# Kernel tuning notes

Hardware: AMD Instinct MI355X
Metric: run time of the kernel (lower is better)

Reference implementation:

```python
import jax, jax.numpy as jnp
import numpy as np

N, E, T, D, A = 50000, 160000, 8192, 32, 6  # nodes, edges, torsions, dim, action_dim


def setup_inputs() -> dict:
    key = jax.random.key(0)
    ks = jax.random.split(key, 16)
    rn = lambda k, s, sc=0.1: jax.random.normal(k, s, jnp.float32) * sc
    return {
        "x": jax.random.normal(ks[0], (N, 3), jnp.float32),
        "edge_index": jax.random.randint(ks[1], (2, E), 0, N),
        "edge_attr": jax.random.uniform(ks[2], (E, 7), dtype=jnp.float32),
        "nonring": jax.random.randint(ks[3], (T, 4), 0, N),
        "lin0_w": rn(ks[4], (3, D)), "lin0_b": jnp.zeros((D,), jnp.float32),
        "nn1_w": rn(ks[5], (7, D)), "nn1_b": jnp.zeros((D,), jnp.float32),
        "nn2_w": rn(ks[6], (D, D * D), 0.02), "nn2_b": jnp.zeros((D * D,), jnp.float32),
        "conv_root": rn(ks[7], (D, D)), "conv_b": jnp.zeros((D,), jnp.float32),
        "gru_w_ih": rn(ks[8], (D, 3 * D)), "gru_w_hh": rn(ks[9], (D, 3 * D)),
        "gru_b_ih": jnp.zeros((3 * D,), jnp.float32), "gru_b_hh": jnp.zeros((3 * D,), jnp.float32),
        "lstm_w_ih": rn(ks[10], (2 * D, 4 * D)), "lstm_w_hh": rn(ks[11], (D, 4 * D)),
        "lstm_b_ih": jnp.zeros((4 * D,), jnp.float32), "lstm_b_hh": jnp.zeros((4 * D,), jnp.float32),
        "lin1_w": rn(ks[12], (6 * D, D)), "lin1_b": jnp.zeros((D,), jnp.float32),
        "lin2_w": rn(ks[13], (D, A)), "lin2_b": jnp.zeros((A,), jnp.float32),
    }


def reference(x, edge_index, edge_attr, nonring,
              lin0_w, lin0_b, nn1_w, nn1_b, nn2_w, nn2_b, conv_root, conv_b,
              gru_w_ih, gru_w_hh, gru_b_ih, gru_b_hh,
              lstm_w_ih, lstm_w_hh, lstm_b_ih, lstm_b_hh,
              lin1_w, lin1_b, lin2_w, lin2_b):
    src, dst = edge_index[0], edge_index[1]
    out = jax.nn.relu(x @ lin0_w + lin0_b)                       # [N, D]
    h = out                                                      # GRU hidden (batch = nodes)
    # Per-edge dim x dim weight matrices (edge_attr is loop-invariant)
    Wedge = (jax.nn.relu(edge_attr @ nn1_w + nn1_b) @ nn2_w + nn2_b).reshape(E, D, D)
    deg = jnp.clip(jax.ops.segment_sum(jnp.ones((E,), jnp.float32), dst, num_segments=N), 1.0)[:, None]
    for _ in range(6):
        # NNConv: gather -> per-edge matvec -> scatter-mean, plus root transform + bias
        msg = jnp.einsum('ei,eio->eo', out[src], Wedge)          # [E, D]
        agg = jax.ops.segment_sum(msg, dst, num_segments=N) / deg
        m = jax.nn.relu(out @ conv_root + agg + conv_b)
        # GRU step (torch gate order r, z, n)
        gx = m @ gru_w_ih + gru_b_ih
        gh = h @ gru_w_hh + gru_b_hh
        r = jax.nn.sigmoid(gx[:, :D] + gh[:, :D])
        z = jax.nn.sigmoid(gx[:, D:2 * D] + gh[:, D:2 * D])
        n = jnp.tanh(gx[:, 2 * D:] + r * gh[:, 2 * D:])
        h = (1.0 - z) * n + z * h
        out = h
    # Set2Set pooling, single graph (B = 1); torch LSTM gate order i, f, g, o
    hl = jnp.zeros((D,), out.dtype)
    cl = jnp.zeros((D,), out.dtype)
    q_star = jnp.zeros((2 * D,), out.dtype)
    for _ in range(6):
        g = q_star @ lstm_w_ih + lstm_b_ih + hl @ lstm_w_hh + lstm_b_hh
        i = jax.nn.sigmoid(g[:D]); f = jax.nn.sigmoid(g[D:2 * D])
        gg = jnp.tanh(g[2 * D:3 * D]); o = jax.nn.sigmoid(g[3 * D:])
        cl = f * cl + i * gg
        hl = o * jnp.tanh(cl)
        q = hl
        a = jax.nn.softmax(out @ q)                              # attention over all nodes
        r_vec = a @ out                                          # [D]
        q_star = jnp.concatenate([q, r_vec])                     # [2D]
    pool = q_star                                                # [2D]
    g4 = out[nonring.reshape(-1)]                                # [4T, D]
    g4 = g4.reshape(4 * D, -1).T                                 # [T, 4D] (faithful view+permute)
    rep = jnp.repeat(pool, g4.shape[0]).reshape(g4.shape[0], -1) # [T, 2D] (repeat_interleave+view)
    cat = jnp.concatenate([g4, rep], axis=1)                     # [T, 6D]
    y = jax.nn.relu(cat @ lin1_w + lin1_b)
    return y @ lin2_w + lin2_b                                   # [T, A]
```

## Files before the change

### kernel.cpp

```cpp
#include <hip/hip_runtime.h>
#include <hip/hip_bf16.h>

#define NN 50000
#define NE 160000
#define NT 8192
#define DD 32
#define AA 6

typedef __attribute__((ext_vector_type(8))) short bf16x8s;
typedef __attribute__((ext_vector_type(4))) float f32x4;

__device__ float g_out[NN * DD];
__device__ float g_msg[NE * DD];
__device__ unsigned int g_h2b[NE * 16];
__device__ int g_src[NE];
__device__ int g_poe[NE];
__device__ unsigned int g_bcnt[NN];
__device__ unsigned int g_row[NN + 1];
__device__ unsigned int g_cur[NN];
__device__ unsigned int g_btot[256], g_boff[256];
__device__ bf16x8s g_w2frag[33 * 2 * 64];
__device__ bf16x8s g_gru_frag[28 * 64];
__device__ float g_hl[DD], g_cl[DD], g_q[DD], g_part[DD + 1];
__device__ unsigned int g_cnt;

__device__ __forceinline__ float sigm(float x) { return 1.0f / (1.0f + __expf(-x)); }
__device__ __forceinline__ float tanhx(float x) { return 1.0f - 2.0f / (__expf(2.0f * x) + 1.0f); }
__device__ __forceinline__ unsigned short f2bf(float f) {
    unsigned int u = __float_as_uint(f);
    u = (u + 0x7fffu + ((u >> 16) & 1u)) >> 16;
    return (unsigned short)u;
}
__device__ __forceinline__ float bflo(unsigned int pk) { return __uint_as_float(pk << 16); }
__device__ __forceinline__ float bfhi(unsigned int pk) { return __uint_as_float(pk & 0xffff0000u); }
__device__ __forceinline__ void fma4(float4& a, float s, const float4 b) {
    a.x = fmaf(s, b.x, a.x); a.y = fmaf(s, b.y, a.y);
    a.z = fmaf(s, b.z, a.z); a.w = fmaf(s, b.w, a.w);
}
#define CVTPK(dst, lo, hi) asm("v_cvt_pk_bf16_f32 %0, %1, %2" : "=v"(dst) : "v"(lo), "v"(hi))

__device__ __forceinline__ void split8(const float* v, bf16x8s& hi, bf16x8s& lo) {
    union U { bf16x8s v; unsigned int u[4]; } H, L;
    CVTPK(H.u[0], v[0], v[1]); CVTPK(H.u[1], v[2], v[3]);
    CVTPK(H.u[2], v[4], v[5]); CVTPK(H.u[3], v[6], v[7]);
    float r[8];
#pragma unroll
    for (int q = 0; q < 4; ++q) {
        r[2 * q]     = v[2 * q]     - bflo(H.u[q]);
        r[2 * q + 1] = v[2 * q + 1] - bfhi(H.u[q]);
    }
    CVTPK(L.u[0], r[0], r[1]); CVTPK(L.u[1], r[2], r[3]);
    CVTPK(L.u[2], r[4], r[5]); CVTPK(L.u[3], r[6], r[7]);
    hi = H.v; lo = L.v;
}

__global__ __launch_bounds__(256) void k_prep0(const float* __restrict__ x,
                                               const float* __restrict__ l0w,
                                               const float* __restrict__ l0b,
                                               const float* __restrict__ w2m,
                                               const float* __restrict__ b2m,
                                               const float* __restrict__ root,
                                               const float* __restrict__ wih,
                                               const float* __restrict__ whh,
                                               const float* __restrict__ lbih,
                                               const float* __restrict__ lbhh) {
    const int t = blockIdx.x * 256 + threadIdx.x;
    {
        const int n = t >> 5, d = t & 31;
        float v = l0b[d];
        v = fmaf(x[n * 3 + 0], l0w[0 * DD + d], v);
        v = fmaf(x[n * 3 + 1], l0w[1 * DD + d], v);
        v = fmaf(x[n * 3 + 2], l0w[2 * DD + d], v);
        g_out[t] = fmaxf(v, 0.f);
    }
    if (t < NN) g_bcnt[t] = 0u;
    if (t < 33 * 2 * 64 * 8) {
        const int j = t & 7, l = (t >> 3) & 63, c = (t >> 9) & 1, s = t >> 10;
        const int kk = (l >> 4) * 8 + j;
        const int col = c * 16 + (l & 15);
        const float v = (s == 32) ? b2m[kk * DD + col] : w2m[(32 * s + kk) * DD + col];
        ((unsigned short*)g_w2frag)[t] = f2bf(v);
    }
    if (t < 28 * 64) {
        const int lane = t & 63, f = t >> 6;
        const float* M; int ncols, c, part;
        if (f < 4)       { M = root; ncols = 32; c = f >> 1;        part = f & 1; }
        else if (f < 16) { M = wih;  ncols = 96; c = (f - 4) >> 1;  part = f & 1; }
        else             { M = whh;  ncols = 96; c = (f - 16) >> 1; part = f & 1; }
        unsigned short out8[8];
#pragma unroll
        for (int j = 0; j < 8; ++j) {
            const int k = (lane >> 4) * 8 + j;
            const float v = M[k * ncols + c * 16 + (lane & 15)];
            const unsigned short hi = f2bf(v);
            out8[j] = (part == 0) ? hi : f2bf(v - __uint_as_float((unsigned int)hi << 16));
        }
        g_gru_frag[f * 64 + lane] = *(bf16x8s*)out8;
    }
    if (t < DD) {
        const float ig = sigm(lbih[t] + lbhh[t]);
        const float g2 = tanhx(lbih[2 * DD + t] + lbhh[2 * DD + t]);
        const float og = sigm(lbih[3 * DD + t] + lbhh[3 * DD + t]);
        const float cc = ig * g2;
        g_cl[t] = cc; const float hn = og * tanhx(cc); g_hl[t] = hn; g_q[t] = hn;
    }
    if (t >= DD && t < 2 * DD + 1 + DD) { if (t - DD <= 2 * DD) g_part[t - DD] = 0.f; }
    if (t == 1793) g_cnt = 0u;
}

__global__ __launch_bounds__(256) void k_hist(const int* __restrict__ ei) {
    const int e = blockIdx.x * 256 + threadIdx.x;
    atomicAdd(&g_bcnt[ei[NE + e]], 1u);
}

__global__ __launch_bounds__(256) void k_scanA() {
    __shared__ unsigned int s[256];
    const int t = threadIdx.x;
    const int idx = blockIdx.x * 256 + t;
    const unsigned int c = (idx < NN) ? g_bcnt[idx] : 0u;
    s[t] = c;
    __syncthreads();
#pragma unroll
    for (int off = 1; off < 256; off <<= 1) {
        const unsigned int o = (t >= off) ? s[t - off] : 0u;
        __syncthreads();
        s[t] += o;
        __syncthreads();
    }
    if (idx < NN) g_row[idx] = s[t] - c;
    if (t == 255) g_btot[blockIdx.x] = s[255];
}

__global__ void k_scanB() {
    __shared__ unsigned int s[256];
    const int t = threadIdx.x;
    const unsigned int c = (t < 196) ? g_btot[t] : 0u;
    s[t] = c;
    __syncthreads();
#pragma unroll
    for (int off = 1; off < 256; off <<= 1) {
        const unsigned int o = (t >= off) ? s[t - off] : 0u;
        __syncthreads();
        s[t] += o;
        __syncthreads();
    }
    if (t < 196) g_boff[t] = s[t] - c;
}

__global__ __launch_bounds__(256) void k_scanC() {
    const int idx = blockIdx.x * 256 + threadIdx.x;
    if (idx < NN) {
        const unsigned int v = g_row[idx] + g_boff[blockIdx.x];
        g_row[idx] = v;
        g_cur[idx] = v;
    }
    if (idx == 0) g_row[NN] = NE;
}

__global__ __launch_bounds__(256) void k_scatter(const int* __restrict__ ei) {
    const int e = blockIdx.x * 256 + threadIdx.x;
    const int d = ei[NE + e];
    const unsigned int pos = atomicAdd(&g_cur[d], 1u);
    g_src[pos] = ei[e];
    g_poe[pos] = e;
}

__global__ __launch_bounds__(256) void k_h2(const float* __restrict__ ea,
                                            const float* __restrict__ w,
                                            const float* __restrict__ b) {
    const int t = blockIdx.x * 256 + threadIdx.x;
    const int p = t >> 4, kp = t & 15;
    const int oe = g_poe[p];
    const int k0 = kp * 2;
    float a0 = b[k0], a1 = b[k0 + 1];
#pragma unroll
    for (int i = 0; i < 7; ++i) {
        const float eav = ea[oe * 7 + i];
        a0 = fmaf(eav, w[i * DD + k0], a0);
        a1 = fmaf(eav, w[i * DD + k0 + 1], a1);
    }
    unsigned int pk;
    CVTPK(pk, fmaxf(a0, 0.f), fmaxf(a1, 0.f));
    g_h2b[t] = pk;
}

__global__ __launch_bounds__(256) void k_edge_mfma() {
    const int wid = threadIdx.x >> 6, lane = threadIdx.x & 63;
    const int w = blockIdx.x * 4 + wid;
    const int col = lane & 15, quad = lane >> 4;
    const bf16x8s* __restrict__ B = g_w2frag;

    const bf16x8s bbias0 = B[32 * 128 + lane];
    const bf16x8s bbias1 = B[32 * 128 + 64 + lane];

    float4 u0[2], u1[2];
    unsigned int h2p[2][16];
#pragma unroll
    for (int g = 0; g < 2; ++g) {
        const int e = w * 32 + g * 16 + col;
        const int src = g_src[e];
        u0[g] = *(const float4*)&g_out[src * DD + quad * 8];
        u1[g] = *(const float4*)&g_out[src * DD + quad * 8 + 4];
        *(uint4*)&h2p[g][0]  = *(const uint4*)&g_h2b[e * 16];
        *(uint4*)&h2p[g][4]  = *(const uint4*)&g_h2b[e * 16 + 4];
        *(uint4*)&h2p[g][8]  = *(const uint4*)&g_h2b[e * 16 + 8];
        *(uint4*)&h2p[g][12] = *(const uint4*)&g_h2b[e * 16 + 12];
    }

    union ABu { bf16x8s v; unsigned int u[4]; };
    f32x4 acc[2][2];
#pragma unroll
    for (int g = 0; g < 2; ++g) {
        acc[g][0] = (f32x4){0.f, 0.f, 0.f, 0.f};
        acc[g][1] = (f32x4){0.f, 0.f, 0.f, 0.f};
    }

#define EDGE_STEP(S, B0V, B1V)                                                                   \
    do {                                                                                          \
        _Pragma("unroll")                                                                         \
        for (int g = 0; g < 2; ++g) {                                                             \
            const unsigned int hw = h2p[g][(S) >> 1];                                             \
            const float hs = ((S)&1) ? bfhi(hw) : bflo(hw);                                       \
            ABu A;                                                                                \
            CVTPK(A.u[0], hs * u0[g].x, hs * u0[g].y);                                            \
            CVTPK(A.u[1], hs * u0[g].z, hs * u0[g].w);                                            \
            CVTPK(A.u[2], hs * u1[g].x, hs * u1[g].y);                                            \
            CVTPK(A.u[3], hs * u1[g].z, hs * u1[g].w);                                            \
            acc[g][0] = __builtin_amdgcn_mfma_f32_16x16x32_bf16(A.v, B0V, acc[g][0], 0, 0, 0);    \
            acc[g][1] = __builtin_amdgcn_mfma_f32_16x16x32_bf16(A.v, B1V, acc[g][1], 0, 0, 0);    \
        }                                                                                         \
    } while (0)

    bf16x8s ca0 = B[0 * 128 + lane], cb0 = B[0 * 128 + 64 + lane];
    bf16x8s ca1 = B[1 * 128 + lane], cb1 = B[1 * 128 + 64 + lane];
    bf16x8s ca2 = B[2 * 128 + lane], cb2 = B[2 * 128 + 64 + lane];
    bf16x8s ca3 = B[3 * 128 + lane], cb3 = B[3 * 128 + 64 + lane];
    bf16x8s na0, nb0, na1, nb1, na2, nb2, na3, nb3;

#pragma unroll
    for (int blk = 0; blk < 8; ++blk) {
        if (blk < 7) {
            const int r = blk * 4 + 4;
            na0 = B[(r + 0) * 128 + lane]; nb0 = B[(r + 0) * 128 + 64 + lane];
            na1 = B[(r + 1) * 128 + lane]; nb1 = B[(r + 1) * 128 + 64 + lane];
            na2 = B[(r + 2) * 128 + lane]; nb2 = B[(r + 2) * 128 + 64 + lane];
            na3 = B[(r + 3) * 128 + lane]; nb3 = B[(r + 3) * 128 + 64 + lane];
        }
        EDGE_STEP(blk * 4 + 0, ca0, cb0);
        EDGE_STEP(blk * 4 + 1, ca1, cb1);
        EDGE_STEP(blk * 4 + 2, ca2, cb2);
        EDGE_STEP(blk * 4 + 3, ca3, cb3);
        if (blk < 7) {
            ca0 = na0; cb0 = nb0; ca1 = na1; cb1 = nb1;
            ca2 = na2; cb2 = nb2; ca3 = na3; cb3 = nb3;
        }
    }
#undef EDGE_STEP

    {
#pragma unroll
        for (int g = 0; g < 2; ++g) {
            ABu Au;
            CVTPK(Au.u[0], u0[g].x, u0[g].y); CVTPK(Au.u[1], u0[g].z, u0[g].w);
            CVTPK(Au.u[2], u1[g].x, u1[g].y); CVTPK(Au.u[3], u1[g].z, u1[g].w);
            acc[g][0] = __builtin_amdgcn_mfma_f32_16x16x32_bf16(Au.v, bbias0, acc[g][0], 0, 0, 0);
            acc[g][1] = __builtin_amdgcn_mfma_f32_16x16x32_bf16(Au.v, bbias1, acc[g][1], 0, 0, 0);
        }
    }
#pragma unroll
    for (int g = 0; g < 2; ++g)
#pragma unroll
        for (int r = 0; r < 4; ++r) {
            const int p = w * 32 + g * 16 + quad * 4 + r;
            g_msg[p * DD + col] = acc[g][0][r];
            g_msg[p * DD + 16 + col] = acc[g][1][r];
        }
}

__global__ __launch_bounds__(256) void k_node_mfma(const float* __restrict__ cb,
                                                   const float* __restrict__ bih,
                                                   const float* __restrict__ bhh) {
    __shared__ float sm[4][16 * 36];
    __shared__ float smsg[4][16 * 32];
    const int wid = threadIdx.x >> 6, lane = threadIdx.x & 63;
    const int nt = blockIdx.x * 4 + wid;
    if (nt >= NN / 16) return;
    const int nb = nt * 16;
    const int col = lane & 15, quad = lane >> 4;
    const bf16x8s* FB = g_gru_frag;
    float* smt = sm[wid];
    float* smm = smsg[wid];

    float hv8[8];
    *(float4*)&hv8[0] = *(const float4*)&g_out[(nb + col) * DD + quad * 8];
    *(float4*)&hv8[4] = *(const float4*)&g_out[(nb + col) * DD + quad * 8 + 4];
    bf16x8s hAh, hAl; split8(hv8, hAh, hAl);

    unsigned int nr0[4], nr1[4];
#pragma unroll
    for (int r = 0; r < 4; ++r) {
        const int node = nb + quad * 4 + r;
        nr0[r] = g_row[node];
        nr1[r] = g_row[node + 1];
    }
    const unsigned int e0t = g_row[nb], e1t = g_row[nb + 16];

    float agg0[4] = {0.f, 0.f, 0.f, 0.f};
    float agg1[4] = {0.f, 0.f, 0.f, 0.f};
    for (unsigned int ec = e0t; ec < e1t; ec += 16) {
        const int idx = min((int)ec * 32 + lane * 8, NE * 32 - 8);
        const float4 v0 = *(const float4*)&g_msg[idx];
        const float4 v1 = *(const float4*)&g_msg[idx + 4];
        *(float4*)&smm[lane * 8] = v0;
        *(float4*)&smm[lane * 8 + 4] = v1;
#pragma unroll
        for (int r = 0; r < 4; ++r) {
            const int lo = (int)max(nr0[r], ec) - (int)ec;
            const int hi = (int)min(nr1[r], ec + 16u) - (int)ec;
            for (int s = lo; s < hi; ++s) {
                agg0[r] += smm[s * 32 + col];
                agg1[r] += smm[s * 32 + 16 + col];
            }
        }
    }

    float invr[4];
#pragma unroll
    for (int r = 0; r < 4; ++r)
        invr[r] = 1.0f / fmaxf((float)(nr1[r] - nr0[r]), 1.0f);

#pragma unroll
    for (int c = 0; c < 2; ++c) {
        const float cbv = cb[c * 16 + col];
        f32x4 aM;
#pragma unroll
        for (int r = 0; r < 4; ++r)
            aM[r] = fmaf((c == 0) ? agg0[r] : agg1[r], invr[r], cbv);
        const bf16x8s Bh = FB[(c * 2 + 0) * 64 + lane];
        const bf16x8s Bl = FB[(c * 2 + 1) * 64 + lane];
        aM = __builtin_amdgcn_mfma_f32_16x16x32_bf16(hAh, Bh, aM, 0, 0, 0);
        aM = __builtin_amdgcn_mfma_f32_16x16x32_bf16(hAl, Bh, aM, 0, 0, 0);
        aM = __builtin_amdgcn_mfma_f32_16x16x32_bf16(hAh, Bl, aM, 0, 0, 0);
#pragma unroll
        for (int r = 0; r < 4; ++r)
            smt[(quad * 4 + r) * 36 + c * 16 + col] = fmaxf(aM[r], 0.f);
    }

    float mv8[8];
    *(float4*)&mv8[0] = *(const float4*)&smt[col * 36 + quad * 8];
    *(float4*)&mv8[4] = *(const float4*)&smt[col * 36 + quad * 8 + 4];
    bf16x8s mAh, mAl; split8(mv8, mAh, mAl);

    f32x4 R[2], Z[2], XN[2], HN[2];
#pragma unroll
    for (int c = 0; c < 6; ++c) {
        const float bx = bih[c * 16 + col], bh = bhh[c * 16 + col];
        f32x4 aX = {bx, bx, bx, bx}, aH = {bh, bh, bh, bh};
        const bf16x8s WIhf = FB[(4 + c * 2) * 64 + lane];
        const bf16x8s WIlf = FB[(5 + c * 2) * 64 + lane];
        const bf16x8s WHhf = FB[(16 + c * 2) * 64 + lane];
        const bf16x8s WHlf = FB[(17 + c * 2) * 64 + lane];
        aX = __builtin_amdgcn_mfma_f32_16x16x32_bf16(mAh, WIhf, aX, 0, 0, 0);
        aX = __builtin_amdgcn_mfma_f32_16x16x32_bf16(mAl, WIhf, aX, 0, 0, 0);
        aX = __builtin_amdgcn_mfma_f32_16x16x32_bf16(mAh, WIlf, aX, 0, 0, 0);
        aH = __builtin_amdgcn_mfma_f32_16x16x32_bf16(hAh, WHhf, aH, 0, 0, 0);
        aH = __builtin_amdgcn_mfma_f32_16x16x32_bf16(hAl, WHhf, aH, 0, 0, 0);
        aH = __builtin_amdgcn_mfma_f32_16x16x32_bf16(hAh, WHlf, aH, 0, 0, 0);
        if (c < 2) {
#pragma unroll
            for (int r = 0; r < 4; ++r) R[c][r] = sigm(aX[r] + aH[r]);
        } else if (c < 4) {
#pragma unroll
            for (int r = 0; r < 4; ++r) Z[c - 2][r] = sigm(aX[r] + aH[r]);
        } else {
            XN[c - 4] = aX; HN[c - 4] = aH;
        }
    }
#pragma unroll
    for (int c = 0; c < 2; ++c)
#pragma unroll
        for (int r = 0; r < 4; ++r) {
            const int addr = (nb + quad * 4 + r) * DD + c * 16 + col;
            const float nv = tanhx(XN[c][r] + R[c][r] * HN[c][r]);
            const float hv = g_out[addr];
            g_out[addr] = (1.f - Z[c][r]) * nv + Z[c][r] * hv;
        }
}

__global__ __launch_bounds__(256) void k_att_f(const float* __restrict__ wih,
                                               const float* __restrict__ whh,
                                               const float* __restrict__ bih,
                                               const float* __restrict__ bhh,
                                               const int dolstm) {
    __shared__ float sq[DD];
    __shared__ float red[4][DD + 1];
    __shared__ int slast;
    __shared__ float qs[64], shl[DD], gg[128];
    if (threadIdx.x < DD) sq[threadIdx.x] = g_q[threadIdx.x];
    __syncthreads();
    float pe = 0.f;
    float pv[DD];
#pragma unroll
    for (int i = 0; i < DD; ++i) pv[i] = 0.f;
    for (int n = blockIdx.x * blockDim.x + threadIdx.x; n < NN; n += gridDim.x * blockDim.x) {
        float row[DD];
#pragma unroll
        for (int q = 0; q < 8; ++q) *(float4*)&row[4 * q] = *(const float4*)&g_out[n * DD + 4 * q];
        float dot = 0.f;
#pragma unroll
        for (int i = 0; i < DD; ++i) dot = fmaf(row[i], sq[i], dot);
        const float e = __expf(dot);
        pe += e;
#pragma unroll
        for (int i = 0; i < DD; ++i) pv[i] = fmaf(e, row[i], pv[i]);
    }
#pragma unroll
    for (int off = 32; off > 0; off >>= 1) {
        pe += __shfl_down(pe, off, 64);
#pragma unroll
        for (int i = 0; i < DD; ++i) pv[i] += __shfl_down(pv[i], off, 64);
    }
    const int wid = threadIdx.x >> 6, lane = threadIdx.x & 63;
    if (lane == 0) {
        red[wid][0] = pe;
#pragma unroll
        for (int i = 0; i < DD; ++i) red[wid][1 + i] = pv[i];
    }
    __syncthreads();
    if (threadIdx.x < DD + 1) {
        const float s = red[0][threadIdx.x] + red[1][threadIdx.x] + red[2][threadIdx.x] + red[3][threadIdx.x];
        atomicAdd(&g_part[threadIdx.x], s);
    }
    __threadfence();
    __syncthreads();
    if (threadIdx.x == 0) {
        const unsigned int o = atomicAdd(&g_cnt, 1u);
        slast = (o == (unsigned int)(gridDim.x - 1)) ? 1 : 0;
    }
    __syncthreads();
    if (!slast) return;
    __threadfence();
    const int t = threadIdx.x;
    if (dolstm) {
        if (t < DD) { qs[t] = g_q[t]; shl[t] = g_hl[t]; }
        else if (t < 64) qs[t] = g_part[1 + t - DD] / g_part[0];
        __syncthreads();
        if (t < 128) {
            float acc = bih[t] + bhh[t];
            for (int i = 0; i < 64; ++i) acc = fmaf(qs[i], wih[i * 128 + t], acc);
            for (int i = 0; i < DD; ++i) acc = fmaf(shl[i], whh[i * 128 + t], acc);
            gg[t] = acc;
        }
        __syncthreads();
        if (t < DD) {
            const float ig = sigm(gg[t]), fg = sigm(gg[DD + t]);
            const float g2 = tanhx(gg[2 * DD + t]), og = sigm(gg[3 * DD + t]);
            const float cc = fmaf(fg, g_cl[t], ig * g2);
            g_cl[t] = cc; const float hn = og * tanhx(cc); g_hl[t] = hn; g_q[t] = hn;
        }
        if (t >= DD && t < 2 * DD + 1) g_part[t - DD] = 0.f;
    }
    if (t == 0) g_cnt = 0u;
}

__global__ __launch_bounds__(128) void k_readout(const int* __restrict__ nr,
                                                 const float* __restrict__ w1,
                                                 const float* __restrict__ b1,
                                                 const float* __restrict__ w2,
                                                 const float* __restrict__ b2,
                                                 float* __restrict__ yout) {
    __shared__ float sw1[192 * DD];
    __shared__ float sS1[DD];
    __shared__ float sw2[DD * AA];
    __shared__ float sb1[DD];
    __shared__ float sb2[AA];
    __shared__ float sred[32 * DD];
    for (int i = threadIdx.x; i < 192 * DD; i += 128) sw1[i] = w1[i];
    for (int i = threadIdx.x; i < DD * AA; i += 128) sw2[i] = w2[i];
    if (threadIdx.x < DD) sb1[threadIdx.x] = b1[threadIdx.x];
    if (threadIdx.x >= DD && threadIdx.x < DD + AA) sb2[threadIdx.x - DD] = b2[threadIdx.x - DD];
    __syncthreads();
    if (threadIdx.x < DD) {
        float s = 0.f;
        for (int c = 0; c < 64; ++c) s += sw1[(128 + c) * DD + threadIdx.x];
        sS1[threadIdx.x] = s;
    }
    __syncthreads();
    const int g = blockIdx.x;
    const int t0 = g * 32;
    const int f = threadIdx.x & 31;
    const int slice = threadIdx.x >> 5;
    const int rowbase = g >> 2, col = g & 3;
    float4 acc[8];
#pragma unroll
    for (int q = 0; q < 8; ++q) acc[q] = make_float4(0.f, 0.f, 0.f, 0.f);
    for (int pp = 0; pp < 32; ++pp) {
        const int p = slice * 32 + pp;
        const int node = nr[(p * 64 + rowbase) * 4 + col];
        const float v = g_out[node * DD + f];
#pragma unroll
        for (int q = 0; q < 8; ++q) fma4(acc[q], v, *(const float4*)&sw1[p * DD + 4 * q]);
    }
#pragma unroll
    for (int q = 0; q < 8; ++q) {
        acc[q].x += __shfl_xor(acc[q].x, 32, 64);
        acc[q].y += __shfl_xor(acc[q].y, 32, 64);
        acc[q].z += __shfl_xor(acc[q].z, 32, 64);
        acc[q].w += __shfl_xor(acc[q].w, 32, 64);
    }
    if (threadIdx.x >= 64 && threadIdx.x < 96) {
#pragma unroll
        for (int q = 0; q < 8; ++q) *(float4*)&sred[f * DD + 4 * q] = acc[q];
    }
    __syncthreads();
    if (threadIdx.x < 32) {
        const int pidx = g >> 2;
        const float poolv = (pidx < DD) ? g_q[pidx] : (g_part[1 + (pidx - DD)] / g_part[0]);
        float y[AA];
#pragma unroll
        for (int a = 0; a < AA; ++a) y[a] = sb2[a];
#pragma unroll
        for (int q = 0; q < 8; ++q) {
            const float4 o = *(const float4*)&sred[f * DD + 4 * q];
            const float vals[4] = {acc[q].x + o.x, acc[q].y + o.y, acc[q].z + o.z, acc[q].w + o.w};
#pragma unroll
            for (int cc = 0; cc < 4; ++cc) {
                const int d = 4 * q + cc;
                const float ad = fmaxf(fmaf(poolv, sS1[d], sb1[d]) + vals[cc], 0.f);
#pragma unroll
                for (int a = 0; a < AA; ++a) y[a] = fmaf(ad, sw2[d * AA + a], y[a]);
            }
        }
#pragma unroll
        for (int a = 0; a < AA; ++a) yout[(t0 + f) * AA + a] = y[a];
    }
}

extern "C" void kernel_launch(void* const* d_in, const int* in_sizes, int n_in,
                              void* d_out, int out_size, void* d_ws, size_t ws_size,
                              hipStream_t stream) {
    (void)in_sizes; (void)n_in; (void)out_size; (void)d_ws; (void)ws_size;
    const float* x        = (const float*)d_in[0];
    const int*   ei       = (const int*)d_in[1];
    const float* ea       = (const float*)d_in[2];
    const int*   nonring  = (const int*)d_in[3];
    const float* lin0_w   = (const float*)d_in[4];
    const float* lin0_b   = (const float*)d_in[5];
    const float* nn1_w    = (const float*)d_in[6];
    const float* nn1_b    = (const float*)d_in[7];
    const float* nn2_w    = (const float*)d_in[8];
    const float* nn2_b    = (const float*)d_in[9];
    const float* conv_root= (const float*)d_in[10];
    const float* conv_b   = (const float*)d_in[11];
    const float* gru_w_ih = (const float*)d_in[12];
    const float* gru_w_hh = (const float*)d_in[13];
    const float* gru_b_ih = (const float*)d_in[14];
    const float* gru_b_hh = (const float*)d_in[15];
    const float* lstm_w_ih= (const float*)d_in[16];
    const float* lstm_w_hh= (const float*)d_in[17];
    const float* lstm_b_ih= (const float*)d_in[18];
    const float* lstm_b_hh= (const float*)d_in[19];
    const float* lin1_w   = (const float*)d_in[20];
    const float* lin1_b   = (const float*)d_in[21];
    const float* lin2_w   = (const float*)d_in[22];
    const float* lin2_b   = (const float*)d_in[23];
    float* out = (float*)d_out;

    k_prep0<<<(NN * DD) / 256, 256, 0, stream>>>(x, lin0_w, lin0_b, nn2_w, nn2_b,
                                                 conv_root, gru_w_ih, gru_w_hh,
                                                 lstm_b_ih, lstm_b_hh);
    k_hist<<<NE / 256, 256, 0, stream>>>(ei);
    k_scanA<<<196, 256, 0, stream>>>();
    k_scanB<<<1, 256, 0, stream>>>();
    k_scanC<<<196, 256, 0, stream>>>();
    k_scatter<<<NE / 256, 256, 0, stream>>>(ei);
    k_h2<<<(NE * 16) / 256, 256, 0, stream>>>(ea, nn1_w, nn1_b);

    for (int it = 0; it < 6; ++it) {
        k_edge_mfma<<<1250, 256, 0, stream>>>();
        k_node_mfma<<<(NN / 16 + 3) / 4, 256, 0, stream>>>(conv_b, gru_b_ih, gru_b_hh);
    }
    for (int s = 0; s < 6; ++s) {
        k_att_f<<<196, 256, 0, stream>>>(lstm_w_ih, lstm_w_hh, lstm_b_ih, lstm_b_hh, (s < 5) ? 1 : 0);
    }
    k_readout<<<256, 128, 0, stream>>>(nonring, lin1_w, lin1_b, lin2_w, lin2_b, out);
}
```

Baseline: 406.5 us.

## Fuse six Set2Set attention launches into one persistent kernel with spin barrier

Replaces six separate attention/LSTM kernel launches with one persistent kernel of 196 blocks that loops over the six Set2Set steps. The blocks wait on a generation counter that the last-arriving block bumps after it computes the LSTM update. Per-step query and partial-sum buffers are indexed by step so no reset is needed between steps. This aims to remove launch gaps and per-launch overhead, at the cost of a software grid barrier that relies on all 196 blocks being resident at once.

```diff
diff --git a/kernel.cpp b/kernel.cpp
--- a/kernel.cpp
+++ b/kernel.cpp
@@ -21,8 +21,11 @@
 __device__ unsigned int g_btot[256], g_boff[256];
 __device__ bf16x8s g_w2frag[33 * 2 * 64];
 __device__ bf16x8s g_gru_frag[28 * 64];
-__device__ float g_hl[DD], g_cl[DD], g_q[DD], g_part[DD + 1];
-__device__ unsigned int g_cnt;
+__device__ float g_hl[DD], g_cl[DD];
+__device__ float g_qs[6][DD];
+__device__ float g_parts[6][DD + 1];
+__device__ unsigned int g_done[8];
+__device__ unsigned int g_gen;
 
 __device__ __forceinline__ float sigm(float x) { return 1.0f / (1.0f + __expf(-x)); }
 __device__ __forceinline__ float tanhx(float x) { return 1.0f - 2.0f / (__expf(2.0f * x) + 1.0f); }
@@ -38,6 +41,8 @@
     a.z = fmaf(s, b.z, a.z); a.w = fmaf(s, b.w, a.w);
 }
 #define CVTPK(dst, lo, hi) asm("v_cvt_pk_bf16_f32 %0, %1, %2" : "=v"(dst) : "v"(lo), "v"(hi))
+#define ALOAD(p)     __hip_atomic_load((p), __ATOMIC_RELAXED, __HIP_MEMORY_SCOPE_AGENT)
+#define ASTORE(p, v) __hip_atomic_store((p), (v), __ATOMIC_RELAXED, __HIP_MEMORY_SCOPE_AGENT)
 
 __device__ __forceinline__ void split8(const float* v, bf16x8s& hi, bf16x8s& lo) {
     union U { bf16x8s v; unsigned int u[4]; } H, L;
@@ -102,10 +107,12 @@
         const float g2 = tanhx(lbih[2 * DD + t] + lbhh[2 * DD + t]);
         const float og = sigm(lbih[3 * DD + t] + lbhh[3 * DD + t]);
         const float cc = ig * g2;
-        g_cl[t] = cc; const float hn = og * tanhx(cc); g_hl[t] = hn; g_q[t] = hn;
-    }
-    if (t >= DD && t < 2 * DD + 1 + DD) { if (t - DD <= 2 * DD) g_part[t - DD] = 0.f; }
-    if (t == 1793) g_cnt = 0u;
+        g_cl[t] = cc; const float hn = og * tanhx(cc); g_hl[t] = hn;
+        ASTORE(&g_qs[0][t], hn);
+    }
+    if (t < 6 * (DD + 1)) ASTORE(&((float*)g_parts)[t], 0.f);
+    if (t >= 512 && t < 520) g_done[t - 512] = 0u;
+    if (t == 520) ASTORE(&g_gen, 0u);
 }
 
 __global__ __launch_bounds__(256) void k_hist(const int* __restrict__ ei) {
@@ -387,80 +394,94 @@
         }
 }
 
-__global__ __launch_bounds__(256) void k_att_f(const float* __restrict__ wih,
-                                               const float* __restrict__ whh,
-                                               const float* __restrict__ bih,
-                                               const float* __restrict__ bhh,
-                                               const int dolstm) {
+__global__ __launch_bounds__(256) void k_s2s_spin(const float* __restrict__ wih,
+                                                  const float* __restrict__ whh,
+                                                  const float* __restrict__ bih,
+                                                  const float* __restrict__ bhh) {
     __shared__ float sq[DD];
     __shared__ float red[4][DD + 1];
     __shared__ int slast;
     __shared__ float qs[64], shl[DD], gg[128];
-    if (threadIdx.x < DD) sq[threadIdx.x] = g_q[threadIdx.x];
-    __syncthreads();
-    float pe = 0.f;
-    float pv[DD];
-#pragma unroll
-    for (int i = 0; i < DD; ++i) pv[i] = 0.f;
-    for (int n = blockIdx.x * blockDim.x + threadIdx.x; n < NN; n += gridDim.x * blockDim.x) {
-        float row[DD];
-#pragma unroll
-        for (int q = 0; q < 8; ++q) *(float4*)&row[4 * q] = *(const float4*)&g_out[n * DD + 4 * q];
-        float dot = 0.f;
-#pragma unroll
-        for (int i = 0; i < DD; ++i) dot = fmaf(row[i], sq[i], dot);
-        const float e = __expf(dot);
-        pe += e;
-#pragma unroll
-        for (int i = 0; i < DD; ++i) pv[i] = fmaf(e, row[i], pv[i]);
-    }
-#pragma unroll
-    for (int off = 32; off > 0; off >>= 1) {
-        pe += __shfl_down(pe, off, 64);
-#pragma unroll
-        for (int i = 0; i < DD; ++i) pv[i] += __shfl_down(pv[i], off, 64);
-    }
-    const int wid = threadIdx.x >> 6, lane = threadIdx.x & 63;
-    if (lane == 0) {
-        red[wid][0] = pe;
-#pragma unroll
-        for (int i = 0; i < DD; ++i) red[wid][1 + i] = pv[i];
-    }
-    __syncthreads();
-    if (threadIdx.x < DD + 1) {
-        const float s = red[0][threadIdx.x] + red[1][threadIdx.x] + red[2][threadIdx.x] + red[3][threadIdx.x];
-        atomicAdd(&g_part[threadIdx.x], s);
-    }
-    __threadfence();
-    __syncthreads();
-    if (threadIdx.x == 0) {
-        const unsigned int o = atomicAdd(&g_cnt, 1u);
-        slast = (o == (unsigned int)(gridDim.x - 1)) ? 1 : 0;
-    }
-    __syncthreads();
-    if (!slast) return;
-    __threadfence();
-    const int t = threadIdx.x;
-    if (dolstm) {
-        if (t < DD) { qs[t] = g_q[t]; shl[t] = g_hl[t]; }
-        else if (t < 64) qs[t] = g_part[1 + t - DD] / g_part[0];
-        __syncthreads();
-        if (t < 128) {
-            float acc = bih[t] + bhh[t];
-            for (int i = 0; i < 64; ++i) acc = fmaf(qs[i], wih[i * 128 + t], acc);
-            for (int i = 0; i < DD; ++i) acc = fmaf(shl[i], whh[i * 128 + t], acc);
-            gg[t] = acc;
-        }
-        __syncthreads();
-        if (t < DD) {
-            const float ig = sigm(gg[t]), fg = sigm(gg[DD + t]);
-            const float g2 = tanhx(gg[2 * DD + t]), og = sigm(gg[3 * DD + t]);
-            const float cc = fmaf(fg, g_cl[t], ig * g2);
-            g_cl[t] = cc; const float hn = og * tanhx(cc); g_hl[t] = hn; g_q[t] = hn;
-        }
-        if (t >= DD && t < 2 * DD + 1) g_part[t - DD] = 0.f;
-    }
-    if (t == 0) g_cnt = 0u;
+    const int lwid = threadIdx.x >> 6, lane = threadIdx.x & 63;
+
+    for (int s = 0; s < 6; ++s) {
+        if (threadIdx.x == 0) {
+            while ((int)__hip_atomic_load(&g_gen, __ATOMIC_ACQUIRE, __HIP_MEMORY_SCOPE_AGENT) < s)
+                __builtin_amdgcn_s_sleep(8);
+        }
+        __syncthreads();
+        if (threadIdx.x < DD) sq[threadIdx.x] = ALOAD(&g_qs[s][threadIdx.x]);
+        __syncthreads();
+
+        float pe = 0.f;
+        float pv[DD];
+#pragma unroll
+        for (int i = 0; i < DD; ++i) pv[i] = 0.f;
+        for (int n = blockIdx.x * 256 + threadIdx.x; n < NN; n += gridDim.x * 256) {
+            float row[DD];
+#pragma unroll
+            for (int q = 0; q < 8; ++q) *(float4*)&row[4 * q] = *(const float4*)&g_out[n * DD + 4 * q];
+            float dot = 0.f;
+#pragma unroll
+            for (int i = 0; i < DD; ++i) dot = fmaf(row[i], sq[i], dot);
+            const float e = __expf(dot);
+            pe += e;
+#pragma unroll
+            for (int i = 0; i < DD; ++i) pv[i] = fmaf(e, row[i], pv[i]);
+        }
+#pragma unroll
+        for (int off = 32; off > 0; off >>= 1) {
+            pe += __shfl_down(pe, off, 64);
+#pragma unroll
+            for (int i = 0; i < DD; ++i) pv[i] += __shfl_down(pv[i], off, 64);
+        }
+        if (lane == 0) {
+            red[lwid][0] = pe;
+#pragma unroll
+            for (int i = 0; i < DD; ++i) red[lwid][1 + i] = pv[i];
+        }
+        __syncthreads();
+        if (threadIdx.x < DD + 1) {
+            const float sv = red[0][threadIdx.x] + red[1][threadIdx.x] + red[2][threadIdx.x] + red[3][threadIdx.x];
+            atomicAdd(&g_parts[s][threadIdx.x], sv);
+        }
+        __threadfence();
+        __syncthreads();
+        if (threadIdx.x == 0) {
+            const unsigned int o = atomicAdd(&g_done[s], 1u);
+            slast = (o == (unsigned int)(gridDim.x - 1)) ? 1 : 0;
+        }
+        __syncthreads();
+
+        if (slast && s < 5) {
+            __threadfence();
+            const int t = threadIdx.x;
+            if (t < DD) { qs[t] = sq[t]; shl[t] = ALOAD(&g_hl[t]); }
+            else if (t < 64) qs[t] = ALOAD(&g_parts[s][1 + t - DD]) / ALOAD(&g_parts[s][0]);
+            __syncthreads();
+            if (t < 128) {
+                float acc = bih[t] + bhh[t];
+                for (int i = 0; i < 64; ++i) acc = fmaf(qs[i], wih[i * 128 + t], acc);
+                for (int i = 0; i < DD; ++i) acc = fmaf(shl[i], whh[i * 128 + t], acc);
+                gg[t] = acc;
+            }
+            __syncthreads();
+            if (t < DD) {
+                const float ig = sigm(gg[t]), fg = sigm(gg[DD + t]);
+                const float g2 = tanhx(gg[2 * DD + t]), og = sigm(gg[3 * DD + t]);
+                const float cc = fmaf(fg, ALOAD(&g_cl[t]), ig * g2);
+                ASTORE(&g_cl[t], cc);
+                const float hn = og * tanhx(cc);
+                ASTORE(&g_hl[t], hn);
+                ASTORE(&g_qs[s + 1][t], hn);
+            }
+            __threadfence();
+            __syncthreads();
+            if (t == 0)
+                __hip_atomic_store(&g_gen, (unsigned int)(s + 1), __ATOMIC_RELEASE,
+                                   __HIP_MEMORY_SCOPE_AGENT);
+        }
+    }
 }
 
 __global__ __launch_bounds__(128) void k_readout(const int* __restrict__ nr,
@@ -515,7 +536,8 @@
     __syncthreads();
     if (threadIdx.x < 32) {
         const int pidx = g >> 2;
-        const float poolv = (pidx < DD) ? g_q[pidx] : (g_part[1 + (pidx - DD)] / g_part[0]);
+        const float poolv = (pidx < DD) ? g_qs[5][pidx]
+                                        : (g_parts[5][1 + (pidx - DD)] / g_parts[5][0]);
         float y[AA];
 #pragma unroll
         for (int a = 0; a < AA; ++a) y[a] = sb2[a];
@@ -580,8 +602,8 @@
         k_edge_mfma<<<1250, 256, 0, stream>>>();
         k_node_mfma<<<(NN / 16 + 3) / 4, 256, 0, stream>>>(conv_b, gru_b_ih, gru_b_hh);
     }
-    for (int s = 0; s < 6; ++s) {
-        k_att_f<<<196, 256, 0, stream>>>(lstm_w_ih, lstm_w_hh, lstm_b_ih, lstm_b_hh, (s < 5) ? 1 : 0);
-    }
+
+    k_s2s_spin<<<196, 256, 0, stream>>>(lstm_w_ih, lstm_w_hh, lstm_b_ih, lstm_b_hh);
+
     k_readout<<<256, 128, 0, stream>>>(nonring, lin1_w, lin1_b, lin2_w, lin2_b, out);
 }
```

Result: slower. 939.3 us (+131.1%).
